# Kernel optimization log

Hardware: AMD Instinct MI355X
Metric: run time of the kernel (lower is better)

## Reference

```python
import jax, jax.numpy as jnp
import numpy as np

B = 16384          # batch
N_IN = 1024        # input nodes
L = 8              # layers
W_LAYER = 512      # nodes per layer (fan-in and fan-out)
N_NODES = N_IN + L * W_LAYER  # 5120 total nodes in shared buffer
MASK_DENSITY = 0.25


def setup_inputs() -> dict:
    key = jax.random.key(0)
    kx, kw, km, kb = jax.random.split(key, 4)
    x = jax.random.normal(kx, (B, N_IN), dtype=jnp.float32)
    W = jax.random.normal(kw, (L, W_LAYER, W_LAYER), dtype=jnp.float32) * 0.05
    mask = (jax.random.uniform(km, (L, W_LAYER, W_LAYER)) < MASK_DENSITY).astype(jnp.float32)
    bias = jax.random.normal(kb, (L, W_LAYER), dtype=jnp.float32) * 0.01
    rng = np.random.default_rng(0)
    # layer l gathers from nodes already computed: indices in [0, N_IN + l*W_LAYER)
    in_idx = np.stack([rng.integers(0, N_IN + l * W_LAYER, size=W_LAYER) for l in range(L)]).astype(np.int32)
    # layer l writes its own contiguous node slots
    out_idx = np.stack([np.arange(N_IN + l * W_LAYER, N_IN + (l + 1) * W_LAYER) for l in range(L)]).astype(np.int32)
    return {"x": x, "W": W, "mask": mask, "bias": bias,
            "in_idx": jnp.asarray(in_idx), "out_idx": jnp.asarray(out_idx)}


def reference(x, W, mask, bias, in_idx, out_idx):
    # shared node-value buffer, inputs written into first N_IN columns
    values = jnp.zeros((x.shape[0], N_NODES), dtype=x.dtype)
    values = values.at[:, :N_IN].set(x)

    def step(vals, layer):
        idx_in, idx_out, Wl, ml, bl = layer
        node_inputs = vals[:, idx_in]                       # [B, W_LAYER] gather
        h = jax.nn.relu(node_inputs @ (Wl * ml).T + bl)     # masked linear + ReLU
        return vals.at[:, idx_out].set(h), None             # scatter back

    values, _ = jax.lax.scan(step, values, (in_idx, out_idx, W, mask, bias))
    return values[:, out_idx[-1]]  # output nodes = last layer's nodes
```

## Files before the change

### kernel.cpp

```cpp
#include <hip/hip_runtime.h>
#include <stdint.h>

typedef unsigned short u16;
typedef unsigned int   u32;
typedef short s16x8 __attribute__((ext_vector_type(8)));
typedef float f32x4 __attribute__((ext_vector_type(4)));

#define NB    16384
#define NIN   1024
#define WLY   512
#define NLAY  8
#define NNODE (NIN + NLAY * WLY)
#define BN    64

__device__ __forceinline__ u16 f2bf(float f) {
  union { float f; u32 u; } c; c.f = f;
  return (u16)((c.u + 0x7fffu + ((c.u >> 16) & 1u)) >> 16);
}
__device__ __forceinline__ float bf2f(u16 h) {
  union { u32 u; float f; } c; c.u = ((u32)h) << 16;
  return c.f;
}

#define SCHED0() __builtin_amdgcn_sched_barrier(0)
#define BAR()    __builtin_amdgcn_s_barrier()
#define WAITVM_IMPL(N) asm volatile("s_waitcnt vmcnt(" #N ")" ::: "memory")
#define WAITVM(N) WAITVM_IMPL(N)
#define WAITLG()  asm volatile("s_waitcnt lgkmcnt(0)" ::: "memory")

__global__ void prep_w(const float* __restrict__ W, const float* __restrict__ Mk,
                       u16* __restrict__ Wm) {
  int id   = blockIdx.x * 256 + threadIdx.x;
  int lane = id & 63;
  int chunk = id >> 6;
  int kf = chunk & 1;
  int mb = (chunk >> 1) & 31;
  int kt = (chunk >> 6) & 7;
  int l  = chunk >> 9;
  int m  = (mb << 4) + (lane & 15);
  int k0 = (kt << 6) + (kf << 5) + ((lane >> 4) << 3);
  size_t base = ((size_t)l << 18) + (size_t)m * 512 + k0;
  const float4* w4 = (const float4*)(W + base);
  const float4* k4 = (const float4*)(Mk + base);
  float4 w0 = w4[0], w1 = w4[1];
  float4 k0v = k4[0], k1v = k4[1];
  u32 p0 = (u32)f2bf(w0.x * k0v.x) | ((u32)f2bf(w0.y * k0v.y) << 16);
  u32 p1 = (u32)f2bf(w0.z * k0v.z) | ((u32)f2bf(w0.w * k0v.w) << 16);
  u32 p2 = (u32)f2bf(w1.x * k1v.x) | ((u32)f2bf(w1.y * k1v.y) << 16);
  u32 p3 = (u32)f2bf(w1.z * k1v.z) | ((u32)f2bf(w1.w * k1v.w) << 16);
  uint4 v; v.x = p0; v.y = p1; v.z = p2; v.w = p3;
  *(uint4*)(Wm + ((size_t)chunk << 9) + (lane << 3)) = v;
}

__global__ __launch_bounds__(512, 2) void fused_net(
    const float* __restrict__ x, const u16* __restrict__ Wfrag,
    const float* __restrict__ bias, const int* __restrict__ in_idx,
    u16* __restrict__ V, float* __restrict__ out) {

  __shared__ __align__(16) u16 Graw[4][4096];
  __shared__ __align__(16) u16 Gswz[2][4096];
  __shared__ __align__(16) u16 Ebuf[512 * 72];
  __shared__ int   idx_s[512];
  __shared__ float bias_s[512];

  int t = threadIdx.x;
  int lane = t & 63, w = t >> 6;
  int mlane = lane & 15, g = lane >> 4;
  int n0 = blockIdx.x * BN;

  float* xt = (float*)Ebuf;
  for (int cc = 0; cc < 8; ++cc) {
    #pragma unroll
    for (int it = 0; it < 4; ++it) {
      int cl = t + it * 512;
      int b = cl >> 5, p = cl & 31;
      *(float4*)(xt + b * 128 + (p << 2)) =
          *(const float4*)(x + (size_t)(n0 + b) * 1024 + cc * 128 + (p << 2));
    }
    __syncthreads();
    {
      int c = t >> 2, seg = t & 3;
      u32 p[8];
      #pragma unroll
      for (int i = 0; i < 8; ++i) {
        u16 lo = f2bf(xt[(seg * 16 + 2 * i) * 128 + c]);
        u16 hi = f2bf(xt[(seg * 16 + 2 * i + 1) * 128 + c]);
        p[i] = (u32)lo | ((u32)hi << 16);
      }
      u16* dst = V + (size_t)(cc * 128 + c) * NB + n0 + seg * 16;
      uint4 v0; v0.x = p[0]; v0.y = p[1]; v0.z = p[2]; v0.w = p[3];
      uint4 v1; v1.x = p[4]; v1.y = p[5]; v1.z = p[6]; v1.w = p[7];
      *(uint4*)dst = v0;
      *(uint4*)(dst + 8) = v1;
    }
    __syncthreads();
  }

#define STAGE(KT, R) do {                                                      \
    int k_ = (w << 3) + (lane >> 3);                                           \
    int row_ = idx_s[((KT) << 6) + k_];                                        \
    const u16* src_ = V + (size_t)row_ * NB + n0 + ((lane & 7) << 3);          \
    __builtin_amdgcn_global_load_lds(                                          \
        (const __attribute__((address_space(1))) u32*)src_,                    \
        (__attribute__((address_space(3))) u32*)(&Graw[R][w << 9]), 16, 0, 0); \
  } while (0)

#define LDA(KTN) do {                                                          \
    _Pragma("unroll") for (int mb = 0; mb < 4; ++mb)                           \
    _Pragma("unroll") for (int kf = 0; kf < 2; ++kf)                           \
      a[(KTN) & 1][mb][kf] = *(const s16x8*)(Wl +                              \
          ((size_t)((((KTN) * 32 + (w << 2) + mb) << 1) + kf) << 9) +          \
          (lane << 3));                                                        \
  } while (0)

#define TRANSP(KT) do {                                                        \
    int n_ = t & 63, kc_ = t >> 6;                                             \
    const u16* gb_ = Graw[(KT) & 3];                                           \
    u32 p0_ = (u32)gb_[(kc_ * 8 + 0) * 64 + n_] |                              \
              ((u32)gb_[(kc_ * 8 + 1) * 64 + n_] << 16);                       \
    u32 p1_ = (u32)gb_[(kc_ * 8 + 2) * 64 + n_] |                              \
              ((u32)gb_[(kc_ * 8 + 3) * 64 + n_] << 16);                       \
    u32 p2_ = (u32)gb_[(kc_ * 8 + 4) * 64 + n_] |                              \
              ((u32)gb_[(kc_ * 8 + 5) * 64 + n_] << 16);                       \
    u32 p3_ = (u32)gb_[(kc_ * 8 + 6) * 64 + n_] |                              \
              ((u32)gb_[(kc_ * 8 + 7) * 64 + n_] << 16);                       \
    uint4 vv_; vv_.x = p0_; vv_.y = p1_; vv_.z = p2_; vv_.w = p3_;             \
    *(uint4*)((char*)Gswz[(KT) & 1] + n_ * 128 +                               \
              ((kc_ * 16) ^ ((n_ & 7) << 4))) = vv_;                           \
  } while (0)

#define MM(KT) do {                                                            \
    const char* gs_ = (const char*)Gswz[(KT) & 1];                             \
    _Pragma("unroll") for (int kf = 0; kf < 2; ++kf) {                         \
      s16x8 bfr[4];                                                            \
      _Pragma("unroll") for (int nf = 0; nf < 4; ++nf) {                       \
        int n_ = (nf << 4) + mlane;                                            \
        bfr[nf] = *(const s16x8*)(gs_ + n_ * 128 +                             \
                  (((kf << 6) + (g << 4)) ^ ((n_ & 7) << 4)));                 \
      }                                                                        \
      _Pragma("unroll") for (int mb = 0; mb < 4; ++mb)                         \
      _Pragma("unroll") for (int nf = 0; nf < 4; ++nf)                         \
        acc[mb][nf] = __builtin_amdgcn_mfma_f32_16x16x32_bf16(                 \
            a[(KT) & 1][mb][kf], bfr[nf], acc[mb][nf], 0, 0, 0);               \
    }                                                                          \
  } while (0)

#define BODY(KT, VMN, PRE, POST) do {                                          \
    if (PRE) { LDA((KT) + 1); }                                                \
    SCHED0(); WAITVM(VMN); SCHED0();                                           \
    BAR();                                                                     \
    if (POST) { STAGE((KT) + 3, ((KT) + 3) & 3); }                             \
    TRANSP(KT);                                                                \
    SCHED0(); WAITLG(); BAR(); SCHED0();                                       \
    MM(KT);                                                                    \
  } while (0)

  for (int l = 0; l < NLAY; ++l) {
    idx_s[t]  = in_idx[(l << 9) + t];
    bias_s[t] = bias[(l << 9) + t];
    __syncthreads();

    const u16* Wl = Wfrag + ((size_t)l << 18);
    int node_out = NIN + l * WLY;

    f32x4 acc[4][4];
    #pragma unroll
    for (int i = 0; i < 4; ++i)
      #pragma unroll
      for (int j = 0; j < 4; ++j)
        acc[i][j] = (f32x4){0.f, 0.f, 0.f, 0.f};

    s16x8 a[2][4][2];

    STAGE(0, 0); STAGE(1, 1); STAGE(2, 2);
    SCHED0();
    LDA(0);
    SCHED0();

    BODY(0, 8, 1, 1);
    BODY(1, 9, 1, 1);
    BODY(2, 9, 1, 1);
    BODY(3, 9, 1, 1);
    BODY(4, 9, 1, 1);
    BODY(5, 9, 1, 0);
    BODY(6, 8, 1, 0);
    BODY(7, 0, 0, 0);

    if (l < NLAY - 1) {
      #pragma unroll
      for (int mb = 0; mb < 4; ++mb)
        #pragma unroll
        for (int nf = 0; nf < 4; ++nf)
          #pragma unroll
          for (int r = 0; r < 4; ++r) {
            int m = (w << 6) + (mb << 4) + (g << 2) + r;
            int n = (nf << 4) + mlane;
            Ebuf[m * 72 + n] = f2bf(fmaxf(acc[mb][nf][r] + bias_s[m], 0.f));
          }
      #pragma unroll
      for (int it = 0; it < 8; ++it) {
        int row = (w << 6) + (it << 3) + (lane >> 3);
        uint4 vv = *(uint4*)(Ebuf + row * 72 + ((lane & 7) << 3));
        *(uint4*)(V + (size_t)(node_out + row) * NB + n0 + ((lane & 7) << 3)) = vv;
      }
    } else {
      #pragma unroll
      for (int mb = 0; mb < 4; ++mb)
        #pragma unroll
        for (int nf = 0; nf < 4; ++nf)
          #pragma unroll
          for (int r = 0; r < 4; ++r) {
            int m = (w << 6) + (mb << 4) + (g << 2) + r;
            int n = (nf << 4) + mlane;
            Ebuf[m * 66 + n] = f2bf(fmaxf(acc[mb][nf][r] + bias_s[m], 0.f));
          }
      __syncthreads();
      #pragma unroll
      for (int pn = 0; pn < 8; ++pn)
        #pragma unroll
        for (int h = 0; h < 2; ++h) {
          int n = (t >> 6) + (pn << 3);
          int mbase = ((t & 63) << 2) + (h << 8);
          float4 v;
          v.x = bf2f(Ebuf[(mbase + 0) * 66 + n]);
          v.y = bf2f(Ebuf[(mbase + 1) * 66 + n]);
          v.z = bf2f(Ebuf[(mbase + 2) * 66 + n]);
          v.w = bf2f(Ebuf[(mbase + 3) * 66 + n]);
          *(float4*)(out + (size_t)(n0 + n) * 512 + mbase) = v;
        }
    }
  }
#undef STAGE
#undef LDA
#undef TRANSP
#undef MM
#undef BODY
}

extern "C" void kernel_launch(void* const* d_in, const int* in_sizes, int n_in,
                              void* d_out, int out_size, void* d_ws, size_t ws_size,
                              hipStream_t stream) {
  (void)in_sizes; (void)n_in; (void)out_size; (void)ws_size;
  const float* x    = (const float*)d_in[0];
  const float* W    = (const float*)d_in[1];
  const float* Mk   = (const float*)d_in[2];
  const float* bias = (const float*)d_in[3];
  const int*  inidx = (const int*)d_in[4];
  float* out = (float*)d_out;

  char* ws = (char*)d_ws;
  u16* V     = (u16*)ws;
  u16* Wfrag = (u16*)(ws + (size_t)NNODE * NB * 2);

  prep_w<<<dim3(1024), 256, 0, stream>>>(W, Mk, Wfrag);
  fused_net<<<dim3(256), 512, 0, stream>>>(x, Wfrag, bias, inidx, V, out);
}
```

Measured before the change: 123.2 us.

## Replace async LDS gather pipeline with register-staged double-buffered loads

Swaps the 4-deep global_load_lds staging with hand-placed waitcnt and barriers for a register-prefetched gather. Rows are loaded two k-tiles ahead into registers, written to a padded LDS buffer, and transposed into the swizzled buffer, with one __syncthreads per k-tile. Index and bias shared-memory staging is dropped: gather row indices are kept in registers and bias is read directly as float4. This cuts the barrier count and LDS footprint, but it relies on the compiler to schedule the loads, and the extra VGPRs may hurt at two blocks per CU.

```diff
diff --git a/kernel.cpp b/kernel.cpp
--- a/kernel.cpp
+++ b/kernel.cpp
@@ -21,12 +21,6 @@
   union { u32 u; float f; } c; c.u = ((u32)h) << 16;
   return c.f;
 }
-
-#define SCHED0() __builtin_amdgcn_sched_barrier(0)
-#define BAR()    __builtin_amdgcn_s_barrier()
-#define WAITVM_IMPL(N) asm volatile("s_waitcnt vmcnt(" #N ")" ::: "memory")
-#define WAITVM(N) WAITVM_IMPL(N)
-#define WAITLG()  asm volatile("s_waitcnt lgkmcnt(0)" ::: "memory")
 
 __global__ void prep_w(const float* __restrict__ W, const float* __restrict__ Mk,
                        u16* __restrict__ Wm) {
@@ -57,16 +51,16 @@
     const float* __restrict__ bias, const int* __restrict__ in_idx,
     u16* __restrict__ V, float* __restrict__ out) {
 
-  __shared__ __align__(16) u16 Graw[4][4096];
+  __shared__ __align__(16) u16 Graw[2][64 * 72];
   __shared__ __align__(16) u16 Gswz[2][4096];
   __shared__ __align__(16) u16 Ebuf[512 * 72];
-  __shared__ int   idx_s[512];
-  __shared__ float bias_s[512];
 
   int t = threadIdx.x;
   int lane = t & 63, w = t >> 6;
   int mlane = lane & 15, g = lane >> 4;
   int n0 = blockIdx.x * BN;
+  int krow  = (w << 3) + (lane >> 3);
+  int kcol8 = lane & 7;
 
   float* xt = (float*)Ebuf;
   for (int cc = 0; cc < 8; ++cc) {
@@ -96,13 +90,26 @@
     __syncthreads();
   }
 
-#define STAGE(KT, R) do {                                                      \
-    int k_ = (w << 3) + (lane >> 3);                                           \
-    int row_ = idx_s[((KT) << 6) + k_];                                        \
-    const u16* src_ = V + (size_t)row_ * NB + n0 + ((lane & 7) << 3);          \
-    __builtin_amdgcn_global_load_lds(                                          \
-        (const __attribute__((address_space(1))) u32*)src_,                    \
-        (__attribute__((address_space(3))) u32*)(&Graw[R][w << 9]), 16, 0, 0); \
+#define GLD(KT) (*(const uint4*)(V + (size_t)rowv[KT] * NB + n0 + (kcol8 << 3)))
+
+#define STW(KT) do {                                                           \
+    *(uint4*)((char*)Graw[(KT) & 1] + krow * 144 + (kcol8 << 4)) =             \
+        gv[(KT) & 1];                                                          \
+  } while (0)
+
+#define TRANSP(KT) do {                                                        \
+    const u16* gb_ = Graw[(KT) & 1];                                           \
+    u32 p0_ = (u32)gb_[(w * 8 + 0) * 72 + lane] |                              \
+              ((u32)gb_[(w * 8 + 1) * 72 + lane] << 16);                       \
+    u32 p1_ = (u32)gb_[(w * 8 + 2) * 72 + lane] |                              \
+              ((u32)gb_[(w * 8 + 3) * 72 + lane] << 16);                       \
+    u32 p2_ = (u32)gb_[(w * 8 + 4) * 72 + lane] |                              \
+              ((u32)gb_[(w * 8 + 5) * 72 + lane] << 16);                       \
+    u32 p3_ = (u32)gb_[(w * 8 + 6) * 72 + lane] |                              \
+              ((u32)gb_[(w * 8 + 7) * 72 + lane] << 16);                       \
+    uint4 vv_; vv_.x = p0_; vv_.y = p1_; vv_.z = p2_; vv_.w = p3_;             \
+    *(uint4*)((char*)Gswz[(KT) & 1] + lane * 128 +                             \
+              ((w * 16) ^ ((lane & 7) << 4))) = vv_;                           \
   } while (0)
 
 #define LDA(KTN) do {                                                          \
@@ -111,22 +118,6 @@
       a[(KTN) & 1][mb][kf] = *(const s16x8*)(Wl +                              \
           ((size_t)((((KTN) * 32 + (w << 2) + mb) << 1) + kf) << 9) +          \
           (lane << 3));                                                        \
-  } while (0)
-
-#define TRANSP(KT) do {                                                        \
-    int n_ = t & 63, kc_ = t >> 6;                                             \
-    const u16* gb_ = Graw[(KT) & 3];                                           \
-    u32 p0_ = (u32)gb_[(kc_ * 8 + 0) * 64 + n_] |                              \
-              ((u32)gb_[(kc_ * 8 + 1) * 64 + n_] << 16);                       \
-    u32 p1_ = (u32)gb_[(kc_ * 8 + 2) * 64 + n_] |                              \
-              ((u32)gb_[(kc_ * 8 + 3) * 64 + n_] << 16);                       \
-    u32 p2_ = (u32)gb_[(kc_ * 8 + 4) * 64 + n_] |                              \
-              ((u32)gb_[(kc_ * 8 + 5) * 64 + n_] << 16);                       \
-    u32 p3_ = (u32)gb_[(kc_ * 8 + 6) * 64 + n_] |                              \
-              ((u32)gb_[(kc_ * 8 + 7) * 64 + n_] << 16);                       \
-    uint4 vv_; vv_.x = p0_; vv_.y = p1_; vv_.z = p2_; vv_.w = p3_;             \
-    *(uint4*)((char*)Gswz[(KT) & 1] + n_ * 128 +                               \
-              ((kc_ * 16) ^ ((n_ & 7) << 4))) = vv_;                           \
   } while (0)
 
 #define MM(KT) do {                                                            \
@@ -145,20 +136,13 @@
     }                                                                          \
   } while (0)
 
-#define BODY(KT, VMN, PRE, POST) do {                                          \
-    if (PRE) { LDA((KT) + 1); }                                                \
-    SCHED0(); WAITVM(VMN); SCHED0();                                           \
-    BAR();                                                                     \
-    if (POST) { STAGE((KT) + 3, ((KT) + 3) & 3); }                             \
-    TRANSP(KT);                                                                \
-    SCHED0(); WAITLG(); BAR(); SCHED0();                                       \
-    MM(KT);                                                                    \
-  } while (0)
-
   for (int l = 0; l < NLAY; ++l) {
-    idx_s[t]  = in_idx[(l << 9) + t];
-    bias_s[t] = bias[(l << 9) + t];
-    __syncthreads();
+    __syncthreads();
+
+    int rowv[8];
+    #pragma unroll
+    for (int kt = 0; kt < 8; ++kt)
+      rowv[kt] = in_idx[(l << 9) + (kt << 6) + krow];
 
     const u16* Wl = Wfrag + ((size_t)l << 18);
     int node_out = NIN + l * WLY;
@@ -171,32 +155,41 @@
         acc[i][j] = (f32x4){0.f, 0.f, 0.f, 0.f};
 
     s16x8 a[2][4][2];
-
-    STAGE(0, 0); STAGE(1, 1); STAGE(2, 2);
-    SCHED0();
+    uint4 gv[2];
+
+    gv[0] = GLD(0);
     LDA(0);
-    SCHED0();
-
-    BODY(0, 8, 1, 1);
-    BODY(1, 9, 1, 1);
-    BODY(2, 9, 1, 1);
-    BODY(3, 9, 1, 1);
-    BODY(4, 9, 1, 1);
-    BODY(5, 9, 1, 0);
-    BODY(6, 8, 1, 0);
-    BODY(7, 0, 0, 0);
+    STW(0);
+    TRANSP(0);
+    gv[1] = GLD(1);
+    __syncthreads();
+
+    #pragma unroll
+    for (int kt = 0; kt < 8; ++kt) {
+      if (kt + 2 < 8) gv[kt & 1] = GLD(kt + 2);
+      if (kt + 1 < 8) {
+        LDA(kt + 1);
+        STW(kt + 1);
+        TRANSP(kt + 1);
+      }
+      MM(kt);
+      __syncthreads();
+    }
 
     if (l < NLAY - 1) {
       #pragma unroll
-      for (int mb = 0; mb < 4; ++mb)
+      for (int mb = 0; mb < 4; ++mb) {
+        float4 bv = *(const float4*)(bias + (l << 9) + (w << 6) + (mb << 4) + (g << 2));
+        float bvr[4] = {bv.x, bv.y, bv.z, bv.w};
         #pragma unroll
         for (int nf = 0; nf < 4; ++nf)
           #pragma unroll
           for (int r = 0; r < 4; ++r) {
             int m = (w << 6) + (mb << 4) + (g << 2) + r;
             int n = (nf << 4) + mlane;
-            Ebuf[m * 72 + n] = f2bf(fmaxf(acc[mb][nf][r] + bias_s[m], 0.f));
+            Ebuf[m * 72 + n] = f2bf(fmaxf(acc[mb][nf][r] + bvr[r], 0.f));
           }
+      }
       #pragma unroll
       for (int it = 0; it < 8; ++it) {
         int row = (w << 6) + (it << 3) + (lane >> 3);
@@ -205,15 +198,18 @@
       }
     } else {
       #pragma unroll
-      for (int mb = 0; mb < 4; ++mb)
+      for (int mb = 0; mb < 4; ++mb) {
+        float4 bv = *(const float4*)(bias + (l << 9) + (w << 6) + (mb << 4) + (g << 2));
+        float bvr[4] = {bv.x, bv.y, bv.z, bv.w};
         #pragma unroll
         for (int nf = 0; nf < 4; ++nf)
           #pragma unroll
           for (int r = 0; r < 4; ++r) {
             int m = (w << 6) + (mb << 4) + (g << 2) + r;
             int n = (nf << 4) + mlane;
-            Ebuf[m * 66 + n] = f2bf(fmaxf(acc[mb][nf][r] + bias_s[m], 0.f));
+            Ebuf[m * 66 + n] = f2bf(fmaxf(acc[mb][nf][r] + bvr[r], 0.f));
           }
+      }
       __syncthreads();
       #pragma unroll
       for (int pn = 0; pn < 8; ++pn)
@@ -230,11 +226,11 @@
         }
     }
   }
-#undef STAGE
+#undef GLD
+#undef STW
+#undef TRANSP
 #undef LDA
-#undef TRANSP
 #undef MM
-#undef BODY
 }
 
 extern "C" void kernel_launch(void* const* d_in, const int* in_sizes, int n_in,
```

Result: slower. 128.4 us (+4.2%).
